# Performance work log

Measured on AMD Instinct MI355X. Metric: run time of the kernel, lower is better.

The kernel has to match this reference:

```python
import jax, jax.numpy as jnp
import jax.scipy as jsp
import numpy as np

H, W, C = 2048, 2048, 3
SCALE, TRANSLATE, ROTATE, SHEAR = 1.15, 0.15, np.pi / 12, 0.0


def _rotation_matrix(r):
    rx, ry = jnp.cos(r), jnp.sin(r)
    return jnp.array([[rx, ry, 0.0], [-ry, rx, 0.0], [0.0, 0.0, 1.0]])


def _scale_matrix(s):
    return jnp.array([[s, 0.0, 0.0], [0.0, s, 0.0], [0.0, 0.0, 1.0]])


def _shear_matrix(r):
    sh = jnp.tan(r)
    return jnp.array([[1.0, sh, 0.0], [0.0, 1.0, 0.0], [0.0, 0.0, 1.0]])


def _translation_matrix(tx, ty):
    return jnp.array([[1.0, 0.0, tx], [0.0, 1.0, ty], [0.0, 0.0, 1.0]])


def setup_inputs() -> dict:
    key = jax.random.key(0)
    k_img, k1, k2, k3, k4, k5 = jax.random.split(key, 6)
    image = jax.random.normal(k_img, (H, W, C), dtype=jnp.float32)
    # Random affine params exactly as RandomAffine.__call__ samples them.
    scale = jax.random.uniform(k1, minval=1.0, maxval=SCALE)
    tx = jax.random.uniform(k2, minval=-TRANSLATE, maxval=TRANSLATE) * W
    ty = jax.random.uniform(k3, minval=-TRANSLATE, maxval=TRANSLATE) * H
    rotation = jax.random.uniform(k4, minval=-1.0, maxval=1.0) * ROTATE
    shear = jax.random.uniform(k5, minval=-1.0, maxval=1.0) * SHEAR
    matrix = (_rotation_matrix(rotation) @ _scale_matrix(scale)
              @ _shear_matrix(shear) @ _translation_matrix(tx, ty))
    return {"image": image, "matrix": matrix.astype(jnp.float32)}


def _apply_affine(image, matrix):
    h, w, c = image.shape
    dtype = image.dtype
    y = jnp.linspace(-h / 2, h / 2, num=h)
    x = jnp.linspace(-w / 2, w / 2, num=w)
    v = jnp.ones(1)
    ch = jnp.arange(3)
    # (h, w, 1, 3, 4) grid of homogeneous coords [y, x, 1, channel]
    coords = jnp.stack(jnp.meshgrid(y, x, v, ch, indexing='ij'), axis=-1).astype(dtype)
    transform = jnp.eye(4, dtype=dtype).at[:-1, :-1].set(matrix.astype(dtype))
    coords = coords @ transform + jnp.array([h / 2, w / 2, 0.0, 0.0], dtype=dtype)
    # drop the homogeneous slot (index -2), keep (y, x, channel)
    coords = jnp.concatenate([coords[..., :2], coords[..., 3:]], axis=-1)
    # 'h w v c yxc -> yxc (h w v c)'
    coords = coords.reshape(-1, 3).T  # (3, h*w*3)
    out = jsp.ndimage.map_coordinates(
        image, [coords[0], coords[1], coords[2]], order=1, mode='reflect')
    return out.reshape(h, w, c)


def reference(image, matrix):
    return _apply_affine(image, matrix)
```

## Files before the change

### kernel.cpp

```cpp
#include <hip/hip_runtime.h>


#define IMG_H 2048
#define IMG_W 2048
#define TILE  32
#define BBH   52
#define BBW   52
#define BBW3  (BBW * 3)
#define ROWV4 (BBW3 / 4)

__device__ __forceinline__ int reflect2048(int i) {
    int p = i & 4095;
    return (p < 2048) ? p : (4095 - p);
}

__global__ __launch_bounds__(256) void affine_tile_kernel(
    const float* __restrict__ img, const float* __restrict__ Mp,
    float* __restrict__ out)
{
    __shared__ float lds[BBH * BBW3];

    const int tid = threadIdx.x;
    const int tbx = blockIdx.x & 63;
    const int tby = blockIdx.x >> 6;
    const int i0 = tby * TILE, j0 = tbx * TILE;

    const float step = 2048.0f / 2047.0f;
    const float m00 = Mp[0], m01 = Mp[1];
    const float m10 = Mp[3], m11 = Mp[4];
    const float b0 = Mp[6] + 1024.0f, b1 = Mp[7] + 1024.0f;

    const float yv0 = fmaf((float)i0,            step, -1024.0f);
    const float yv1 = fmaf((float)(i0 + TILE-1), step, -1024.0f);
    const float xv0 = fmaf((float)j0,            step, -1024.0f);
    const float xv1 = fmaf((float)(j0 + TILE-1), step, -1024.0f);

    const float rya = yv0*m00 + xv0*m10 + b0, ryb = yv0*m00 + xv1*m10 + b0;
    const float ryc = yv1*m00 + xv0*m10 + b0, ryd = yv1*m00 + xv1*m10 + b0;
    const float rxa = yv0*m01 + xv0*m11 + b1, rxb = yv0*m01 + xv1*m11 + b1;
    const float rxc = yv1*m01 + xv0*m11 + b1, rxd = yv1*m01 + xv1*m11 + b1;

    const float min_ry = fminf(fminf(rya, ryb), fminf(ryc, ryd));
    const float min_rx = fminf(fminf(rxa, rxb), fminf(rxc, rxd));

    const int y0 = (int)floorf(min_ry) - 1;
    const int x0 = ((int)floorf(min_rx) - 1) & ~3;

    if (x0 >= 0 && x0 + BBW <= IMG_W) {
        const int wid = tid >> 6, lane = tid & 63;
        if (lane < ROWV4) {
            #pragma unroll
            for (int r = wid; r < BBH; r += 4) {
                const int gy = reflect2048(y0 + r);
                const float4 v = *(const float4*)(img + gy * (IMG_W*3) + x0*3 + lane*4);
                *(float4*)&lds[r * BBW3 + lane * 4] = v;
            }
        }
    } else {
        for (int e = tid; e < BBH * BBW; e += 256) {
            const int r  = e / BBW;
            const int xx = e - r * BBW;
            const int gy = reflect2048(y0 + r);
            const int gx = reflect2048(x0 + xx);
            const float* s = img + (gy * IMG_W + gx) * 3;
            float* d = &lds[r * BBW3 + xx * 3];
            d[0] = s[0]; d[1] = s[1]; d[2] = s[2];
        }
    }
    __syncthreads();

    #pragma unroll
    for (int r = 0; r < 4; ++r) {
        const int li = r * 8 + (tid >> 5);
        const int lj = tid & 31;
        const int i = i0 + li, j = j0 + lj;

        const float yv = fmaf((float)i, step, -1024.0f);
        const float xv = fmaf((float)j, step, -1024.0f);
        const float ry = yv*m00 + xv*m10 + b0;
        const float rx = yv*m01 + xv*m11 + b1;

        const float fy = floorf(ry), fx = floorf(rx);
        const float wy1 = ry - fy, wx1 = rx - fx;
        const float wy0 = 1.0f - wy1, wx0 = 1.0f - wx1;

        const int iy = (int)fy - y0;
        const int ix = (int)fx - x0;

        const float* p0 = &lds[iy * BBW3 + ix * 3];
        const float* p1 = p0 + BBW3;

        const float w00 = wy0*wx0, w01 = wy0*wx1;
        const float w10 = wy1*wx0, w11 = wy1*wx1;

        const int o = (i * IMG_W + j) * 3;
        out[o + 0] = w00*p0[0] + w01*p0[3] + w10*p1[0] + w11*p1[3];
        out[o + 1] = w00*p0[1] + w01*p0[4] + w10*p1[1] + w11*p1[4];
        out[o + 2] = w00*p0[2] + w01*p0[5] + w10*p1[2] + w11*p1[5];
    }
}

extern "C" void kernel_launch(void* const* d_in, const int* in_sizes, int n_in,
                              void* d_out, int out_size, void* d_ws, size_t ws_size,
                              hipStream_t stream) {
    const float* img = (const float*)d_in[0];
    const float* M   = (const float*)d_in[1];
    float* out = (float*)d_out;

    dim3 grid((IMG_H / TILE) * (IMG_W / TILE)), block(256);
    hipLaunchKernelGGL(affine_tile_kernel, grid, block, 0, stream, img, M, out);
}
```

Baseline: 119.6 us.

## Process four tiles per block with register-prefetched next-tile staging

Each block now handles four horizontally adjacent 32x32 tiles. While computing the current tile from LDS, it prefetches the next tile's bounding box into registers and writes it to LDS after a barrier. The LDS box shrinks to 48x39 float4s. Each thread now computes four consecutive pixels and writes the output as float4 stores. The aim is to hide global load latency and vectorise stores. In exchange it uses more registers, cuts the grid by 4x, and a 48-row box may be too small for some rotations.

Result: slower. 159.7 us (+33.5%).

```diff
diff --git a/kernel.cpp b/kernel.cpp
--- a/kernel.cpp
+++ b/kernel.cpp
@@ -4,26 +4,29 @@
 #define IMG_H 2048
 #define IMG_W 2048
 #define TILE  32
-#define BBH   52
-#define BBW   52
-#define BBW3  (BBW * 3)
-#define ROWV4 (BBW3 / 4)
+#define NT    4
+#define BBH   48
+#define NV4   39
+#define BBW3  (NV4 * 4)
+#define NELEM (BBH * NV4)
+#define PF    8
 
 __device__ __forceinline__ int reflect2048(int i) {
     int p = i & 4095;
     return (p < 2048) ? p : (4095 - p);
 }
 
-__global__ __launch_bounds__(256) void affine_tile_kernel(
+__global__ __launch_bounds__(256) void affine_pipe_kernel(
     const float* __restrict__ img, const float* __restrict__ Mp,
     float* __restrict__ out)
 {
     __shared__ float lds[BBH * BBW3];
 
     const int tid = threadIdx.x;
-    const int tbx = blockIdx.x & 63;
-    const int tby = blockIdx.x >> 6;
-    const int i0 = tby * TILE, j0 = tbx * TILE;
+    const int grp = blockIdx.x & 15;
+    const int tby = blockIdx.x >> 4;
+    const int i0 = tby * TILE;
+    const int j0base = grp * (TILE * NT);
 
     const float step = 2048.0f / 2047.0f;
     const float m00 = Mp[0], m01 = Mp[1];
@@ -32,71 +35,106 @@
 
     const float yv0 = fmaf((float)i0,            step, -1024.0f);
     const float yv1 = fmaf((float)(i0 + TILE-1), step, -1024.0f);
-    const float xv0 = fmaf((float)j0,            step, -1024.0f);
-    const float xv1 = fmaf((float)(j0 + TILE-1), step, -1024.0f);
 
-    const float rya = yv0*m00 + xv0*m10 + b0, ryb = yv0*m00 + xv1*m10 + b0;
-    const float ryc = yv1*m00 + xv0*m10 + b0, ryd = yv1*m00 + xv1*m10 + b0;
-    const float rxa = yv0*m01 + xv0*m11 + b1, rxb = yv0*m01 + xv1*m11 + b1;
-    const float rxc = yv1*m01 + xv0*m11 + b1, rxd = yv1*m01 + xv1*m11 + b1;
+    auto bbox = [&](int j0, int& y0, int& x0, bool& fast) {
+        const float xva = fmaf((float)j0,          step, -1024.0f);
+        const float xvb = fmaf((float)(j0+TILE-1), step, -1024.0f);
+        const float rya = yv0*m00 + xva*m10 + b0, ryb = yv0*m00 + xvb*m10 + b0;
+        const float ryc = yv1*m00 + xva*m10 + b0, ryd = yv1*m00 + xvb*m10 + b0;
+        const float rxa = yv0*m01 + xva*m11 + b1, rxb = yv0*m01 + xvb*m11 + b1;
+        const float rxc = yv1*m01 + xva*m11 + b1, rxd = yv1*m01 + xvb*m11 + b1;
+        y0 = (int)floorf(fminf(fminf(rya,ryb), fminf(ryc,ryd))) - 1;
+        x0 = ((int)floorf(fminf(fminf(rxa,rxb), fminf(rxc,rxd))) - 1) & ~3;
+        fast = (x0 >= 0) && (x0*3 + NV4*4 <= IMG_W*3);
+    };
 
-    const float min_ry = fminf(fminf(rya, ryb), fminf(ryc, ryd));
-    const float min_rx = fminf(fminf(rxa, rxb), fminf(rxc, rxd));
+    float4 pf[PF];
 
-    const int y0 = (int)floorf(min_ry) - 1;
-    const int x0 = ((int)floorf(min_rx) - 1) & ~3;
-
-    if (x0 >= 0 && x0 + BBW <= IMG_W) {
-        const int wid = tid >> 6, lane = tid & 63;
-        if (lane < ROWV4) {
-            #pragma unroll
-            for (int r = wid; r < BBH; r += 4) {
+    auto issue = [&](int y0, int x0) {
+        #pragma unroll
+        for (int k = 0; k < PF; ++k) {
+            const int e = tid + 256*k;
+            if (e < NELEM) {
+                const int r = e / NV4, s = e - r*NV4;
                 const int gy = reflect2048(y0 + r);
-                const float4 v = *(const float4*)(img + gy * (IMG_W*3) + x0*3 + lane*4);
-                *(float4*)&lds[r * BBW3 + lane * 4] = v;
+                pf[k] = *(const float4*)(img + gy*(IMG_W*3) + x0*3 + s*4);
             }
         }
-    } else {
-        for (int e = tid; e < BBH * BBW; e += 256) {
-            const int r  = e / BBW;
-            const int xx = e - r * BBW;
+    };
+    auto writeback = [&]() {
+        #pragma unroll
+        for (int k = 0; k < PF; ++k) {
+            const int e = tid + 256*k;
+            if (e < NELEM) {
+                const int r = e / NV4, s = e - r*NV4;
+                *(float4*)&lds[r*BBW3 + s*4] = pf[k];
+            }
+        }
+    };
+    auto slowfill = [&](int y0, int x0) {
+        for (int e = tid; e < BBH*52; e += 256) {
+            const int r  = e / 52;
+            const int xx = e - r*52;
             const int gy = reflect2048(y0 + r);
             const int gx = reflect2048(x0 + xx);
-            const float* s = img + (gy * IMG_W + gx) * 3;
-            float* d = &lds[r * BBW3 + xx * 3];
+            const float* s = img + (gy*IMG_W + gx)*3;
+            float* d = &lds[r*BBW3 + xx*3];
             d[0] = s[0]; d[1] = s[1]; d[2] = s[2];
         }
-    }
+    };
+
+    auto compute = [&](int j0, int y0, int x0) {
+        const int row = tid >> 3;
+        const int col = (tid & 7) * 4;
+        const int i = i0 + row;
+        const float yv = fmaf((float)i, step, -1024.0f);
+        float v[12];
+        #pragma unroll
+        for (int k = 0; k < 4; ++k) {
+            const float xv = fmaf((float)(j0 + col + k), step, -1024.0f);
+            const float ry = yv*m00 + xv*m10 + b0;
+            const float rx = yv*m01 + xv*m11 + b1;
+            const float fy = floorf(ry), fx = floorf(rx);
+            const float wy1 = ry - fy, wx1 = rx - fx;
+            const float wy0 = 1.0f - wy1, wx0 = 1.0f - wx1;
+            const int iy = (int)fy - y0;
+            const int ix = (int)fx - x0;
+            const float* p0 = &lds[iy*BBW3 + ix*3];
+            const float* p1 = p0 + BBW3;
+            const float w00 = wy0*wx0, w01 = wy0*wx1;
+            const float w10 = wy1*wx0, w11 = wy1*wx1;
+            v[k*3+0] = w00*p0[0] + w01*p0[3] + w10*p1[0] + w11*p1[3];
+            v[k*3+1] = w00*p0[1] + w01*p0[4] + w10*p1[1] + w11*p1[4];
+            v[k*3+2] = w00*p0[2] + w01*p0[5] + w10*p1[2] + w11*p1[5];
+        }
+        float* ob = out + (i*IMG_W + j0 + col)*3;
+        *(float4*)(ob+0) = make_float4(v[0], v[1], v[2],  v[3]);
+        *(float4*)(ob+4) = make_float4(v[4], v[5], v[6],  v[7]);
+        *(float4*)(ob+8) = make_float4(v[8], v[9], v[10], v[11]);
+    };
+
+    int y0c, x0c; bool fastc;
+    bbox(j0base, y0c, x0c, fastc);
+    if (fastc) { issue(y0c, x0c); writeback(); }
+    else       { slowfill(y0c, x0c); }
     __syncthreads();
 
-    #pragma unroll
-    for (int r = 0; r < 4; ++r) {
-        const int li = r * 8 + (tid >> 5);
-        const int lj = tid & 31;
-        const int i = i0 + li, j = j0 + lj;
-
-        const float yv = fmaf((float)i, step, -1024.0f);
-        const float xv = fmaf((float)j, step, -1024.0f);
-        const float ry = yv*m00 + xv*m10 + b0;
-        const float rx = yv*m01 + xv*m11 + b1;
-
-        const float fy = floorf(ry), fx = floorf(rx);
-        const float wy1 = ry - fy, wx1 = rx - fx;
-        const float wy0 = 1.0f - wy1, wx0 = 1.0f - wx1;
-
-        const int iy = (int)fy - y0;
-        const int ix = (int)fx - x0;
-
-        const float* p0 = &lds[iy * BBW3 + ix * 3];
-        const float* p1 = p0 + BBW3;
-
-        const float w00 = wy0*wx0, w01 = wy0*wx1;
-        const float w10 = wy1*wx0, w11 = wy1*wx1;
-
-        const int o = (i * IMG_W + j) * 3;
-        out[o + 0] = w00*p0[0] + w01*p0[3] + w10*p1[0] + w11*p1[3];
-        out[o + 1] = w00*p0[1] + w01*p0[4] + w10*p1[1] + w11*p1[4];
-        out[o + 2] = w00*p0[2] + w01*p0[5] + w10*p1[2] + w11*p1[5];
+    for (int t = 0; t < NT; ++t) {
+        const int j0 = j0base + t*TILE;
+        int y0n, x0n; bool fastn = false;
+        const bool havenext = (t+1 < NT);
+        if (havenext) {
+            bbox(j0 + TILE, y0n, x0n, fastn);
+            if (fastn) issue(y0n, x0n);
+        }
+        compute(j0, y0c, x0c);
+        __syncthreads();
+        if (havenext) {
+            if (fastn) writeback();
+            else       slowfill(y0n, x0n);
+            y0c = y0n; x0c = x0n;
+            __syncthreads();
+        }
     }
 }
 
@@ -107,6 +145,6 @@
     const float* M   = (const float*)d_in[1];
     float* out = (float*)d_out;
 
-    dim3 grid((IMG_H / TILE) * (IMG_W / TILE)), block(256);
-    hipLaunchKernelGGL(affine_tile_kernel, grid, block, 0, stream, img, M, out);
+    dim3 grid((IMG_H / TILE) * (IMG_W / (TILE * NT))), block(256);
+    hipLaunchKernelGGL(affine_pipe_kernel, grid, block, 0, stream, img, M, out);
 }
```
